# Optimization experiments

Hardware: AMD Instinct MI355X
Metric: run time of the kernel (lower is better)

The kernel has to match this reference:

```python
import jax, jax.numpy as jnp
import numpy as np

B, S, DM, DC = 16, 4096, 1280, 768
N_AOE, N_IMG, N_DELTA = 16, 16, 16
ANAT_GATE, DIS_GATE, DELTA_SCALE = 0.5, 0.5, 1.0


def setup_inputs() -> dict:
    key = jax.random.key(0)
    ks = jax.random.split(key, 9)
    def lin(k, fan_in, fan_out):
        return jax.random.normal(k, (fan_in, fan_out), jnp.float32) / np.sqrt(fan_in)
    return {
        "hidden_states": jax.random.normal(ks[0], (B, S, DM), jnp.float32),
        "encoder_hidden_states": jax.random.normal(ks[1], (B, N_AOE + N_IMG + N_DELTA, DC), jnp.float32),
        "w_q": lin(ks[2], DM, DM),
        "w_k": lin(ks[3], DC, DM),
        "w_v": lin(ks[4], DC, DM),
        "w_k_dis": lin(ks[5], DC, DM),
        "w_v_dis": lin(ks[6], DC, DM),
        "w_out": lin(ks[7], DM, DM),
        "b_out": jnp.zeros((DM,), jnp.float32),
        "n_heads": 8,
    }


def _heads(x, h):
    b, s, d = x.shape
    return x.reshape(b, s, h, d // h).transpose(0, 2, 1, 3)  # [B,H,S,dh]


def _attend(q, k, v, scale):
    # q:[B,H,Sq,dh], k/v:[B,H,Sk,dh], Sk small (16)
    scores = jnp.einsum("bhqd,bhkd->bhqk", q, k) * scale
    probs = jax.nn.softmax(scores, axis=-1)
    return jnp.einsum("bhqk,bhkd->bhqd", probs, v)


def reference(hidden_states, encoder_hidden_states, w_q, w_k, w_v,
              w_k_dis, w_v_dis, w_out, b_out, n_heads):
    residual = hidden_states
    dh = DM // n_heads
    scale = 1.0 / np.sqrt(dh)

    dis_tok = encoder_hidden_states[:, :N_AOE, :]
    anat_tok = encoder_hidden_states[:, N_AOE:N_AOE + N_IMG, :]
    delta_tok = encoder_hidden_states[:, -N_DELTA:, :]

    q = _heads(hidden_states @ w_q, n_heads)
    z_anat = _attend(q, _heads(anat_tok @ w_k, n_heads), _heads(anat_tok @ w_v, n_heads), scale)
    z_dis = _attend(q, _heads(dis_tok @ w_k_dis, n_heads), _heads(dis_tok @ w_v_dis, n_heads), scale)
    z_delta = _attend(q, _heads(delta_tok @ w_k_dis, n_heads), _heads(delta_tok @ w_v_dis, n_heads), scale)

    z = ANAT_GATE * z_anat + DIS_GATE * z_dis + DELTA_SCALE * z_delta
    out = z.transpose(0, 2, 1, 3).reshape(hidden_states.shape[0], -1, DM)
    out = out @ w_out + b_out  # to_out[0]; to_out[1] dropout = identity in eval
    return out + residual  # residual_connection, rescale_output_factor=1.0
```

## Files before the change

### kernel.cpp

```cpp
#include <hip/hip_runtime.h>
#include <hip/hip_bf16.h>

#define B_ 16
#define S_ 4096
#define DM_ 1280
#define DC_ 768
#define NC_ 384
#define SCALE_ 0.07905694150420949f

typedef __attribute__((ext_vector_type(8))) short bf16x8;
typedef __attribute__((ext_vector_type(4))) float f32x4;
typedef __attribute__((ext_vector_type(4))) unsigned short u16x4;

#define S_BARRIER() asm volatile("s_barrier" ::: "memory")
#define WAIT_VM(n) asm volatile("s_waitcnt vmcnt(" #n ")" ::: "memory")
#define WAIT_LGKM0() asm volatile("s_waitcnt lgkmcnt(0)" ::: "memory")

__device__ __forceinline__ unsigned short f2bf(float f) {
    unsigned int u = __builtin_bit_cast(unsigned int, f);
    u = (u + 0x7FFFu + ((u >> 16) & 1u)) >> 16;
    return (unsigned short)u;
}

__device__ __forceinline__ bf16x8 pack8(float4 x0, float4 x1) {
    bf16x8 a;
    a[0] = __builtin_bit_cast(short, __float2bfloat16(x0.x));
    a[1] = __builtin_bit_cast(short, __float2bfloat16(x0.y));
    a[2] = __builtin_bit_cast(short, __float2bfloat16(x0.z));
    a[3] = __builtin_bit_cast(short, __float2bfloat16(x0.w));
    a[4] = __builtin_bit_cast(short, __float2bfloat16(x1.x));
    a[5] = __builtin_bit_cast(short, __float2bfloat16(x1.y));
    a[6] = __builtin_bit_cast(short, __float2bfloat16(x1.z));
    a[7] = __builtin_bit_cast(short, __float2bfloat16(x1.w));
    return a;
}

__device__ __forceinline__ void gload16(const void* g, void* l) {
    __builtin_amdgcn_global_load_lds(
        (const __attribute__((address_space(1))) void*)g,
        (__attribute__((address_space(3))) void*)l, 16, 0, 0);
}

__device__ __forceinline__ void tcvt_body(const float* __restrict__ in,
                                          unsigned short* __restrict__ out,
                                          int R, int C, int bx, int by, int tid) {
    __shared__ float tile[32][33];
    int c0 = bx * 32, r0 = by * 32;
    int tx = tid & 31, ty = tid >> 5;
    for (int i = ty; i < 32; i += 8)
        tile[i][tx] = in[(size_t)(r0 + i) * C + c0 + tx];
    __syncthreads();
    for (int i = ty; i < 32; i += 8)
        out[(size_t)(c0 + i) * R + r0 + tx] = f2bf(tile[tx][i]);
}

__global__ __launch_bounds__(256)
void k_prep(const float* __restrict__ wq, const float* __restrict__ wk,
            const float* __restrict__ wv, const float* __restrict__ wkd,
            const float* __restrict__ wvd, const float* __restrict__ wout,
            unsigned short* __restrict__ wq_bf, unsigned short* __restrict__ wTk,
            unsigned short* __restrict__ wTv, unsigned short* __restrict__ wTkd,
            unsigned short* __restrict__ wTvd, unsigned short* __restrict__ woutT) {
    int bid = blockIdx.x, tid = threadIdx.x;
    if (bid < 1600) {
        int i = bid * 256 + tid;
        float4 v = ((const float4*)wq)[i];
        u16x4 o = { f2bf(v.x), f2bf(v.y), f2bf(v.z), f2bf(v.w) };
        ((u16x4*)wq_bf)[i] = o;
    } else if (bid < 2560) {
        int r = bid - 1600; tcvt_body(wk,  wTk,  DC_, DM_, r % 40, r / 40, tid);
    } else if (bid < 3520) {
        int r = bid - 2560; tcvt_body(wv,  wTv,  DC_, DM_, r % 40, r / 40, tid);
    } else if (bid < 4480) {
        int r = bid - 3520; tcvt_body(wkd, wTkd, DC_, DM_, r % 40, r / 40, tid);
    } else if (bid < 5440) {
        int r = bid - 4480; tcvt_body(wvd, wTvd, DC_, DM_, r % 40, r / 40, tid);
    } else {
        int r = bid - 5440; tcvt_body(wout, woutT, DM_, DM_, r % 40, r / 40, tid);
    }
}

__global__ __launch_bounds__(256)
void k_projM(const float* __restrict__ enc,
             const unsigned short* __restrict__ wTk, const unsigned short* __restrict__ wTv,
             const unsigned short* __restrict__ wTkd, const unsigned short* __restrict__ wTvd,
             unsigned short* __restrict__ KV) {
    int bid = blockIdx.x;
    int j = bid / 80, rem = bid % 80, b = rem / 5, nt = rem % 5;
    int tid = threadIdx.x, w = tid >> 6, l = tid & 63, l15 = l & 15, l4 = l >> 4;
    int tok0 = (j < 2) ? 16 : ((j < 4) ? 0 : 32);
    const unsigned short* wT = (j == 0) ? wTk : (j == 1) ? wTv : (j == 2 || j == 4) ? wTkd : wTvd;
    const float* ap = enc + ((size_t)(b * 48 + tok0 + l15)) * DC_;
    f32x4 zero = {0.f, 0.f, 0.f, 0.f};
    f32x4 acc[4];
    #pragma unroll
    for (int t = 0; t < 4; t++) acc[t] = zero;
    for (int kk = 0; kk < 24; kk++) {
        const float4* hp = (const float4*)(ap + kk * 32 + l4 * 8);
        bf16x8 af = pack8(hp[0], hp[1]);
        #pragma unroll
        for (int t = 0; t < 4; t++) {
            int n0 = nt * 256 + w * 64 + t * 16;
            bf16x8 bf = *(const bf16x8*)(wT + (size_t)(n0 + l15) * DC_ + kk * 32 + l4 * 8);
            acc[t] = __builtin_amdgcn_mfma_f32_16x16x32_bf16(af, bf, acc[t], 0, 0, 0);
        }
    }
    #pragma unroll
    for (int t = 0; t < 4; t++) {
        int e = nt * 256 + w * 64 + t * 16 + l15;
        #pragma unroll
        for (int r = 0; r < 4; r++)
            KV[((size_t)(j * 16 + b) * 16 + l4 * 4 + r) * DM_ + e] = f2bf(acc[t][r]);
    }
}

__global__ __launch_bounds__(256)
void k_au(const unsigned short* __restrict__ KV, const unsigned short* __restrict__ wqbf,
          const unsigned short* __restrict__ woutT,
          unsigned short* __restrict__ At2, unsigned short* __restrict__ Ut2) {
    int bid0 = blockIdx.x;
    bool isA = bid0 < 384;
    int bid = isA ? bid0 : bid0 - 384;
    int b = bid & 15, r_ = bid >> 4, x = r_ >> 3, h = r_ & 7;
    int tid = threadIdx.x, w = tid >> 6, l = tid & 63, l15 = l & 15, l4 = l >> 4;
    int xh = x * 8 + h;
    int jrow = isA ? (2 * x) : (2 * x + 1);
    const unsigned short* wmat = isA ? wqbf : woutT;
    float postscale = isA ? SCALE_ : ((x == 2) ? 1.0f : 0.5f);
    bf16x8 bfr[5];
    #pragma unroll
    for (int kk = 0; kk < 5; kk++)
        bfr[kk] = *(const bf16x8*)(KV + ((size_t)(jrow * 16 + b) * 16 + l15) * DM_ + h * 160 + kk * 32 + l4 * 8);
    f32x4 zero = {0.f, 0.f, 0.f, 0.f};
    for (int tt = 0; tt < 20; tt++) {
        int d0 = w * 320 + tt * 16;
        f32x4 acc = zero;
        if (isA) {
            #pragma unroll
            for (int kk = 0; kk < 5; kk++) {
                bf16x8 af = *(const bf16x8*)(wmat + (size_t)(d0 + l15) * DM_ + h * 160 + kk * 32 + l4 * 8);
                acc = __builtin_amdgcn_mfma_f32_16x16x32_bf16(af, bfr[kk], acc, 0, 0, 0);
            }
            int c = xh * 16 + l15;
            u16x4 pk;
            #pragma unroll
            for (int r = 0; r < 4; r++) pk[r] = f2bf(acc[r] * postscale);
            *(u16x4*)(At2 + ((size_t)(b * 40 + (d0 >> 5)) * NC_ + c) * 32 + (d0 & 31) + l4 * 4) = pk;
        } else {
            #pragma unroll
            for (int kk = 0; kk < 5; kk++) {
                bf16x8 af = *(const bf16x8*)(wmat + (size_t)(d0 + l15) * DM_ + h * 160 + kk * 32 + l4 * 8);
                acc = __builtin_amdgcn_mfma_f32_16x16x32_bf16(bfr[kk], af, acc, 0, 0, 0);
            }
            int e = d0 + l15;
            u16x4 pk;
            #pragma unroll
            for (int r = 0; r < 4; r++) pk[r] = f2bf(acc[r] * postscale);
            *(u16x4*)(Ut2 + ((size_t)(b * 12 + (xh >> 1)) * DM_ + e) * 32 + (xh & 1) * 16 + l4 * 4) = pk;
        }
    }
}

__global__ __launch_bounds__(256, 2)
void k_fused(const float* __restrict__ hid, const unsigned short* __restrict__ At2,
             const unsigned short* __restrict__ Ut2, const float* __restrict__ bo,
             float* __restrict__ out) {
    __shared__ char smem[81920];
    unsigned short* Apnl = (unsigned short*)smem;
    char* Hlds = smem + 49152;
    unsigned short* Ulds2 = (unsigned short*)(smem + 49152);
    int bid = blockIdx.x;
    int orig = (bid & 7) * 128 + (bid >> 3);
    int b = orig >> 6, st = orig & 63;
    int s0 = st * 64;
    int tid = threadIdx.x, w = tid >> 6, l = tid & 63, l15 = l & 15, l4 = l >> 4;
    int rdsw = (l4 ^ ((l15 >> 1) & 3)) * 8;
    const unsigned short* Ab = At2 + (size_t)b * 40 * NC_ * 32;
    const float* hsrc = hid + ((size_t)b * S_ + s0) * DM_;
    f32x4 zero = {0.f, 0.f, 0.f, 0.f};

    {
        f32x4 acc[4][6];
        #pragma unroll
        for (int si = 0; si < 4; si++)
            #pragma unroll
            for (int cj = 0; cj < 6; cj++) acc[si][cj] = zero;

        auto stageA = [&](int kk, int ab) {
            const unsigned short* slab = Ab + (size_t)kk * (NC_ * 32);
            #pragma unroll
            for (int i = 0; i < 6; i++) {
                int idx = i * 256 + tid;
                int c = idx >> 2, m = (idx & 3) ^ ((c >> 1) & 3);
                gload16(slab + (size_t)c * 32 + m * 8, smem + ab * 24576 + idx * 16);
            }
        };
        auto stageH = [&](int kk, int hb) {
            #pragma unroll
            for (int i = 0; i < 2; i++) {
                int idx = i * 256 + tid;
                int r = idx >> 3, sg = (idx & 7) ^ (r & 7);
                gload16(hsrc + (size_t)r * DM_ + kk * 32 + sg * 4, Hlds + hb * 8192 + idx * 16);
            }
        };
        auto compute = [&](int ab, int hb) {
            bf16x8 hpk[4];
            #pragma unroll
            for (int si = 0; si < 4; si++) {
                int r = si * 16 + l15;
                float4 lo = *(const float4*)(Hlds + hb * 8192 + r * 128 + (((2 * l4) ^ (l15 & 7)) * 16));
                float4 hi = *(const float4*)(Hlds + hb * 8192 + r * 128 + (((2 * l4 + 1) ^ (l15 & 7)) * 16));
                hpk[si] = pack8(lo, hi);
            }
            __builtin_amdgcn_s_setprio(1);
            #pragma unroll
            for (int cj = 0; cj < 6; cj++) {
                bf16x8 af = *(const bf16x8*)&Apnl[ab * 12288 + (w * 96 + cj * 16 + l15) * 32 + rdsw];
                #pragma unroll
                for (int si = 0; si < 4; si++)
                    acc[si][cj] = __builtin_amdgcn_mfma_f32_16x16x32_bf16(af, hpk[si], acc[si][cj], 0, 0, 0);
            }
            __builtin_amdgcn_s_setprio(0);
        };
        auto SITER = [&](int kk) {
            stageA(kk + 1, (kk + 1) & 1);
            stageH(kk + 2, (kk + 2) % 3);
            WAIT_VM(10);
            S_BARRIER();
            compute(kk & 1, kk % 3);
            WAIT_LGKM0();
            S_BARRIER();
        };

        stageA(0, 0); stageH(0, 0); stageH(1, 1);
        for (int k0 = 0; k0 < 36; k0 += 6) {
            SITER(k0 + 0); SITER(k0 + 1); SITER(k0 + 2);
            SITER(k0 + 3); SITER(k0 + 4); SITER(k0 + 5);
        }
        SITER(36); SITER(37);
        stageA(39, 1);
        WAIT_VM(8);
        S_BARRIER();
        compute(0, 38 % 3);
        WAIT_LGKM0();
        S_BARRIER();
        WAIT_VM(0);
        S_BARRIER();
        compute(1, 39 % 3);
        WAIT_LGKM0();
        S_BARRIER();

        #pragma unroll
        for (int si = 0; si < 4; si++) {
            int s_l = si * 16 + l15;
            #pragma unroll
            for (int cj = 0; cj < 6; cj++) {
                float v0 = acc[si][cj][0], v1 = acc[si][cj][1], v2 = acc[si][cj][2], v3 = acc[si][cj][3];
                float mx = fmaxf(fmaxf(v0, v1), fmaxf(v2, v3));
                mx = fmaxf(mx, __shfl_xor(mx, 16));
                mx = fmaxf(mx, __shfl_xor(mx, 32));
                float e0 = __expf(v0 - mx), e1 = __expf(v1 - mx), e2 = __expf(v2 - mx), e3 = __expf(v3 - mx);
                float sm = e0 + e1 + e2 + e3;
                sm += __shfl_xor(sm, 16);
                sm += __shfl_xor(sm, 32);
                float rs = 1.0f / sm;
                u16x4 pk = { f2bf(e0 * rs), f2bf(e1 * rs), f2bf(e2 * rs), f2bf(e3 * rs) };
                int c = w * 96 + cj * 16 + l4 * 4;
                int chunk = ((c & 31) >> 3) ^ (s_l & 3);
                *(u16x4*)(smem + (c >> 5) * 4096 + s_l * 64 + chunk * 16 + (l4 & 1) * 8) = pk;
            }
        }
    }
    __syncthreads();

    const unsigned short* Ub = Ut2 + (size_t)b * 12 * DM_ * 32;
    auto stageU = [&](int kk2, int ec, int buf) {
        const unsigned short* slab = Ub + ((size_t)kk2 * DM_ + ec * 256) * 32;
        #pragma unroll
        for (int i = 0; i < 4; i++) {
            int idx = i * 256 + tid;
            int r = idx >> 2, m = (idx & 3) ^ ((r >> 1) & 3);
            gload16(slab + (size_t)r * 32 + m * 8, (char*)Ulds2 + buf * 16384 + idx * 16);
        }
    };

    for (int ec = 0; ec < 5; ec++) {
        f32x4 accp[4][4];
        #pragma unroll
        for (int si = 0; si < 4; si++)
            #pragma unroll
            for (int ej = 0; ej < 4; ej++) accp[si][ej] = zero;

        stageU(0, ec, 0);
        for (int kk2 = 0; kk2 < 12; kk2++) {
            if (kk2 < 11) {
                stageU(kk2 + 1, ec, (kk2 + 1) & 1);
                WAIT_VM(4);
            } else {
                WAIT_VM(0);
            }
            S_BARRIER();
            int buf = kk2 & 1;
            bf16x8 uf[4], pf[4];
            #pragma unroll
            for (int ej = 0; ej < 4; ej++)
                uf[ej] = *(const bf16x8*)&Ulds2[buf * 8192 + (w * 64 + ej * 16 + l15) * 32 + rdsw];
            #pragma unroll
            for (int si = 0; si < 4; si++) {
                int s_l = si * 16 + l15;
                pf[si] = *(const bf16x8*)(smem + kk2 * 4096 + s_l * 64 + ((l4 ^ (l15 & 3)) * 16));
            }
            __builtin_amdgcn_s_setprio(1);
            #pragma unroll
            for (int si = 0; si < 4; si++)
                #pragma unroll
                for (int ej = 0; ej < 4; ej++)
                    accp[si][ej] = __builtin_amdgcn_mfma_f32_16x16x32_bf16(uf[ej], pf[si], accp[si][ej], 0, 0, 0);
            __builtin_amdgcn_s_setprio(0);
            WAIT_LGKM0();
            S_BARRIER();
        }

        #pragma unroll
        for (int ej = 0; ej < 4; ej++) {
            int e0c = ec * 256 + w * 64 + ej * 16 + l4 * 4;
            float4 b4 = *(const float4*)(bo + e0c);
            #pragma unroll
            for (int si = 0; si < 4; si++) {
                int srow = s0 + si * 16 + l15;
                size_t off = ((size_t)b * S_ + srow) * DM_ + e0c;
                float4 h4 = *(const float4*)(hid + off);
                f32x4 a = accp[si][ej];
                float4 o4;
                o4.x = a[0] + b4.x + h4.x;
                o4.y = a[1] + b4.y + h4.y;
                o4.z = a[2] + b4.z + h4.z;
                o4.w = a[3] + b4.w + h4.w;
                *(float4*)(out + off) = o4;
            }
        }
    }
}

extern "C" void kernel_launch(void* const* d_in, const int* in_sizes, int n_in,
                              void* d_out, int out_size, void* d_ws, size_t ws_size,
                              hipStream_t stream) {
    const float* hid  = (const float*)d_in[0];
    const float* enc  = (const float*)d_in[1];
    const float* wq   = (const float*)d_in[2];
    const float* wk   = (const float*)d_in[3];
    const float* wv   = (const float*)d_in[4];
    const float* wkd  = (const float*)d_in[5];
    const float* wvd  = (const float*)d_in[6];
    const float* wout = (const float*)d_in[7];
    const float* bo   = (const float*)d_in[8];
    float* out = (float*)d_out;

    char* ws = (char*)d_ws;
    unsigned short* At2    = (unsigned short*)(ws);
    unsigned short* Ut2    = (unsigned short*)(ws + 15728640);
    unsigned short* KV     = (unsigned short*)(ws + 31457280);
    unsigned short* wq_bf  = (unsigned short*)(ws + 35389440);
    unsigned short* woutT  = (unsigned short*)(ws + 38666240);
    unsigned short* wTk    = (unsigned short*)(ws + 41943040);
    unsigned short* wTv    = (unsigned short*)(ws + 43909120);
    unsigned short* wTkd   = (unsigned short*)(ws + 45875200);
    unsigned short* wTvd   = (unsigned short*)(ws + 47841280);

    k_prep<<<7040, 256, 0, stream>>>(wq, wk, wv, wkd, wvd, wout,
                                     wq_bf, wTk, wTv, wTkd, wTvd, woutT);
    k_projM<<<480, 256, 0, stream>>>(enc, wTk, wTv, wTkd, wTvd, KV);
    k_au<<<768, 256, 0, stream>>>(KV, wq_bf, woutT, At2, Ut2);
    k_fused<<<1024, 256, 0, stream>>>(hid, At2, Ut2, bo, out);
}
```

Baseline: 393.8 us.

## Fuse K/V projection into A/U kernel and adjust LDS swizzle

Removes the separate k_projM launch and its KV global buffer. Each k_au2 block now computes its own 16x160 head slice of the K or V projection via MFMA, stores it in shared memory, and reads it from there. This saves a kernel launch and a global round trip, at the cost of some redundancy: each projection slice is recomputed in both the A and U halves and re-reads encoder rows per block. Separately, the LDS XOR swizzle for the probability tile in k_fused now uses (s_l>>1)&3 instead of s_l&3, which is meant to reduce bank conflicts.

```diff
diff --git a/kernel.cpp b/kernel.cpp
--- a/kernel.cpp
+++ b/kernel.cpp
@@ -81,57 +81,54 @@
 }
 
 __global__ __launch_bounds__(256)
-void k_projM(const float* __restrict__ enc,
-             const unsigned short* __restrict__ wTk, const unsigned short* __restrict__ wTv,
-             const unsigned short* __restrict__ wTkd, const unsigned short* __restrict__ wTvd,
-             unsigned short* __restrict__ KV) {
-    int bid = blockIdx.x;
-    int j = bid / 80, rem = bid % 80, b = rem / 5, nt = rem % 5;
-    int tid = threadIdx.x, w = tid >> 6, l = tid & 63, l15 = l & 15, l4 = l >> 4;
-    int tok0 = (j < 2) ? 16 : ((j < 4) ? 0 : 32);
-    const unsigned short* wT = (j == 0) ? wTk : (j == 1) ? wTv : (j == 2 || j == 4) ? wTkd : wTvd;
-    const float* ap = enc + ((size_t)(b * 48 + tok0 + l15)) * DC_;
-    f32x4 zero = {0.f, 0.f, 0.f, 0.f};
-    f32x4 acc[4];
-    #pragma unroll
-    for (int t = 0; t < 4; t++) acc[t] = zero;
-    for (int kk = 0; kk < 24; kk++) {
-        const float4* hp = (const float4*)(ap + kk * 32 + l4 * 8);
-        bf16x8 af = pack8(hp[0], hp[1]);
-        #pragma unroll
-        for (int t = 0; t < 4; t++) {
-            int n0 = nt * 256 + w * 64 + t * 16;
-            bf16x8 bf = *(const bf16x8*)(wT + (size_t)(n0 + l15) * DC_ + kk * 32 + l4 * 8);
-            acc[t] = __builtin_amdgcn_mfma_f32_16x16x32_bf16(af, bf, acc[t], 0, 0, 0);
-        }
-    }
-    #pragma unroll
-    for (int t = 0; t < 4; t++) {
-        int e = nt * 256 + w * 64 + t * 16 + l15;
-        #pragma unroll
-        for (int r = 0; r < 4; r++)
-            KV[((size_t)(j * 16 + b) * 16 + l4 * 4 + r) * DM_ + e] = f2bf(acc[t][r]);
-    }
-}
-
-__global__ __launch_bounds__(256)
-void k_au(const unsigned short* __restrict__ KV, const unsigned short* __restrict__ wqbf,
-          const unsigned short* __restrict__ woutT,
-          unsigned short* __restrict__ At2, unsigned short* __restrict__ Ut2) {
+void k_au2(const float* __restrict__ enc,
+           const unsigned short* __restrict__ wTk, const unsigned short* __restrict__ wTv,
+           const unsigned short* __restrict__ wTkd, const unsigned short* __restrict__ wTvd,
+           const unsigned short* __restrict__ wqbf, const unsigned short* __restrict__ woutT,
+           unsigned short* __restrict__ At2, unsigned short* __restrict__ Ut2) {
+    __shared__ unsigned short kvLds[16 * 168];
     int bid0 = blockIdx.x;
     bool isA = bid0 < 384;
     int bid = isA ? bid0 : bid0 - 384;
     int b = bid & 15, r_ = bid >> 4, x = r_ >> 3, h = r_ & 7;
     int tid = threadIdx.x, w = tid >> 6, l = tid & 63, l15 = l & 15, l4 = l >> 4;
     int xh = x * 8 + h;
-    int jrow = isA ? (2 * x) : (2 * x + 1);
+    int tok0 = (x == 0) ? 16 : ((x == 1) ? 0 : 32);
+    const unsigned short* wTproj = isA ? ((x == 0) ? wTk : wTkd)
+                                       : ((x == 0) ? wTv : wTvd);
     const unsigned short* wmat = isA ? wqbf : woutT;
     float postscale = isA ? SCALE_ : ((x == 2) ? 1.0f : 0.5f);
+    f32x4 zero = {0.f, 0.f, 0.f, 0.f};
+
+    {
+        const float* ap = enc + ((size_t)(b * 48 + tok0 + l15)) * DC_;
+        f32x4 pacc[3];
+        #pragma unroll
+        for (int i = 0; i < 3; i++) pacc[i] = zero;
+        for (int kk = 0; kk < 24; kk++) {
+            const float4* hp = (const float4*)(ap + kk * 32 + l4 * 8);
+            bf16x8 af = pack8(hp[0], hp[1]);
+            int i = 0;
+            for (int t2 = w; t2 < 10; t2 += 4, i++) {
+                int n0 = h * 160 + t2 * 16;
+                bf16x8 bf = *(const bf16x8*)(wTproj + (size_t)(n0 + l15) * DC_ + kk * 32 + l4 * 8);
+                pacc[i] = __builtin_amdgcn_mfma_f32_16x16x32_bf16(af, bf, pacc[i], 0, 0, 0);
+            }
+        }
+        int i = 0;
+        for (int t2 = w; t2 < 10; t2 += 4, i++) {
+            #pragma unroll
+            for (int r = 0; r < 4; r++)
+                kvLds[(l4 * 4 + r) * 168 + t2 * 16 + l15] = f2bf(pacc[i][r]);
+        }
+    }
+    __syncthreads();
+
     bf16x8 bfr[5];
     #pragma unroll
     for (int kk = 0; kk < 5; kk++)
-        bfr[kk] = *(const bf16x8*)(KV + ((size_t)(jrow * 16 + b) * 16 + l15) * DM_ + h * 160 + kk * 32 + l4 * 8);
-    f32x4 zero = {0.f, 0.f, 0.f, 0.f};
+        bfr[kk] = *(const bf16x8*)&kvLds[l15 * 168 + kk * 32 + l4 * 8];
+
     for (int tt = 0; tt < 20; tt++) {
         int d0 = w * 320 + tt * 16;
         f32x4 acc = zero;
@@ -266,7 +263,7 @@
                 float rs = 1.0f / sm;
                 u16x4 pk = { f2bf(e0 * rs), f2bf(e1 * rs), f2bf(e2 * rs), f2bf(e3 * rs) };
                 int c = w * 96 + cj * 16 + l4 * 4;
-                int chunk = ((c & 31) >> 3) ^ (s_l & 3);
+                int chunk = ((c & 31) >> 3) ^ ((s_l >> 1) & 3);
                 *(u16x4*)(smem + (c >> 5) * 4096 + s_l * 64 + chunk * 16 + (l4 & 1) * 8) = pk;
             }
         }
@@ -308,7 +305,7 @@
             #pragma unroll
             for (int si = 0; si < 4; si++) {
                 int s_l = si * 16 + l15;
-                pf[si] = *(const bf16x8*)(smem + kk2 * 4096 + s_l * 64 + ((l4 ^ (l15 & 3)) * 16));
+                pf[si] = *(const bf16x8*)(smem + kk2 * 4096 + s_l * 64 + ((l4 ^ ((s_l >> 1) & 3)) * 16));
             }
             __builtin_amdgcn_s_setprio(1);
             #pragma unroll
@@ -359,17 +356,15 @@
     char* ws = (char*)d_ws;
     unsigned short* At2    = (unsigned short*)(ws);
     unsigned short* Ut2    = (unsigned short*)(ws + 15728640);
-    unsigned short* KV     = (unsigned short*)(ws + 31457280);
-    unsigned short* wq_bf  = (unsigned short*)(ws + 35389440);
-    unsigned short* woutT  = (unsigned short*)(ws + 38666240);
-    unsigned short* wTk    = (unsigned short*)(ws + 41943040);
-    unsigned short* wTv    = (unsigned short*)(ws + 43909120);
-    unsigned short* wTkd   = (unsigned short*)(ws + 45875200);
-    unsigned short* wTvd   = (unsigned short*)(ws + 47841280);
+    unsigned short* wq_bf  = (unsigned short*)(ws + 31457280);
+    unsigned short* woutT  = (unsigned short*)(ws + 34734080);
+    unsigned short* wTk    = (unsigned short*)(ws + 38010880);
+    unsigned short* wTv    = (unsigned short*)(ws + 39976960);
+    unsigned short* wTkd   = (unsigned short*)(ws + 41943040);
+    unsigned short* wTvd   = (unsigned short*)(ws + 43909120);
 
     k_prep<<<7040, 256, 0, stream>>>(wq, wk, wv, wkd, wvd, wout,
                                      wq_bf, wTk, wTv, wTkd, wTvd, woutT);
-    k_projM<<<480, 256, 0, stream>>>(enc, wTk, wTv, wTkd, wTvd, KV);
-    k_au<<<768, 256, 0, stream>>>(KV, wq_bf, woutT, At2, Ut2);
+    k_au2<<<768, 256, 0, stream>>>(enc, wTk, wTv, wTkd, wTvd, wq_bf, woutT, At2, Ut2);
     k_fused<<<1024, 256, 0, stream>>>(hid, At2, Ut2, bo, out);
 }
```

Measured after the change: 400.1 us. About the same (+1.6%).
